# Optimization experiments

Measured on AMD Instinct MI355X. Metric: run time of the kernel, lower is better.

## Reference

```python
import jax, jax.numpy as jnp
import numpy as np

VOCAB, D = 10000, 32
QUEUE_LEN = 100


def setup_inputs() -> dict:
    key = jax.random.key(0)
    ks = jax.random.split(key, 8)
    B, T = 64, 1024
    s = 0.1
    return dict(
        inputs=jax.random.randint(ks[0], (B, T), 0, 10000, dtype=jnp.int32),
        emb=jax.random.normal(ks[1], (VOCAB, D), dtype=jnp.float32) * s,
        k_lstm=jax.random.normal(ks[2], (D, 4 * D), dtype=jnp.float32) * s,
        rk_lstm=jax.random.normal(ks[3], (D, 4 * D), dtype=jnp.float32) * s,
        b_lstm=jnp.zeros((4 * D,), dtype=jnp.float32),
        W1=jax.random.normal(ks[4], (D, D), dtype=jnp.float32) * s,
        b1=jnp.zeros((D,), dtype=jnp.float32),
        W2=jax.random.normal(ks[5], (D, 1), dtype=jnp.float32) * s,
        b2=jnp.zeros((1,), dtype=jnp.float32),
    )


def _lstm(x, k, rk, b):
    # Keras LSTM, gate order [i, f, g(cell), o], sigmoid recurrent act, tanh act.
    B, T, D = x.shape
    xg = jnp.einsum('btd,de->bte', x, k) + b  # precompute input projections

    def step(carry, xg_t):
        h, c = carry
        z = xg_t + h @ rk
        i, f, g, o = jnp.split(z, 4, axis=-1)
        c = jax.nn.sigmoid(f) * c + jax.nn.sigmoid(i) * jnp.tanh(g)
        h = jax.nn.sigmoid(o) * jnp.tanh(c)
        return (h, c), h

    init = (jnp.zeros((B, D), x.dtype), jnp.zeros((B, D), x.dtype))
    _, hs = jax.lax.scan(step, init, jnp.swapaxes(xg, 0, 1))  # [T,B,D]
    return jnp.swapaxes(hs, 0, 1)  # [B,T,D]


def _zero_index_queue(x_ids):
    # Vectorized replacement of the (i,j) Python scan: last QUEUE_LEN positions
    # (row-major order) where token==0, as [QUEUE_LEN,2] int32, padded with -1.
    B, T = x_ids.shape
    flat = (x_ids == 0).reshape(-1)
    N = flat.shape[0]
    ridx = jnp.nonzero(flat[::-1], size=QUEUE_LEN, fill_value=-1)[0]
    pos = jnp.where(ridx >= 0, N - 1 - ridx, -1)[::-1]  # ascending, like deque
    ii = jnp.where(pos >= 0, pos // T, -1)
    jj = jnp.where(pos >= 0, pos % T, -1)
    return jnp.stack([ii, jj], axis=-1).astype(jnp.int32)


def _forward_float(x_ids, emb, k_lstm, rk_lstm, b_lstm, W1, b1, W2, b2):
    x = emb[x_ids]                                  # [B,T,D]
    h = _lstm(x, k_lstm, rk_lstm, b_lstm)           # [B,T,D]
    scores = jnp.einsum('btd,bsd->bts', h, h)       # unscaled dot attention
    attn = jax.nn.softmax(scores, axis=-1)
    ctx = jnp.einsum('bts,bsd->btd', attn, h)       # Keras Attention output
    y = jnp.einsum('btd,bte->bde', ctx, h)          # Dot(axes=(1,1)) -> [B,D,D]
    y = jax.nn.relu(y @ W1 + b1)
    return jax.nn.sigmoid(y @ W2 + b2)              # [B,D,1]


def reference(inputs, emb, k_lstm, rk_lstm, b_lstm, W1, b1, W2, b2):
    x_ids = jnp.where(inputs < VOCAB, inputs, 0)
    out = _forward_float(x_ids, emb, k_lstm, rk_lstm, b_lstm, W1, b1, W2, b2)
    return out, _zero_index_queue(x_ids)
```

## Files before the change

kernel.cpp:

```cpp
#include <hip/hip_runtime.h>
#include <math.h>

#define BB 64
#define TT 1024
#define DD 32
#define GG 128
#define VOCABN 10000
#define QLEN 100

typedef short short8 __attribute__((ext_vector_type(8)));
typedef float floatx4 __attribute__((ext_vector_type(4)));
typedef float floatx2 __attribute__((ext_vector_type(2)));
typedef unsigned short u16;

__device__ __forceinline__ float fsig(float x) {
    return __builtin_amdgcn_rcpf(1.0f + __expf(-x));
}
__device__ __forceinline__ float readlane_f(float v, int l) {
    return __int_as_float(__builtin_amdgcn_readlane(__float_as_int(v), l));
}
__device__ __forceinline__ u16 f2bf_rne(float x) {
    unsigned u = __float_as_uint(x);
    u += 0x7FFF + ((u >> 16) & 1);
    return (u16)(u >> 16);
}
__device__ __forceinline__ float bf2f(u16 s) {
    return __uint_as_float(((unsigned)s) << 16);
}
__device__ __forceinline__ floatx2 fma2(float s, floatx2 w, floatx2 acc) {
    return __builtin_elementwise_fma((floatx2){s, s}, w, acc);
}

#define UU 8
__global__
__attribute__((amdgpu_flat_work_group_size(128, 128)))
__attribute__((amdgpu_waves_per_eu(1, 1)))
void k_lstm_scan(const int* __restrict__ ids,
                 const float* __restrict__ emb,
                 const float* __restrict__ klstm,
                 const float* __restrict__ bias,
                 const float* __restrict__ rk,
                 u16* __restrict__ hh, u16* __restrict__ hl,
                 u16* __restrict__ th, u16* __restrict__ tl,
                 int* __restrict__ list,
                 float* __restrict__ outq) {
    const int b = blockIdx.x;
    const int tid = threadIdx.x;
    const int wv = tid >> 6;
    const int l = tid & 63;
    if (b >= BB) {
        if (wv != 0) return;
        const int4* v4 = (const int4*)ids;
        const int C4 = (BB * TT) / 4 / 64;
        const int b4 = l * C4;
        int cnt = 0;
#pragma unroll 4
        for (int i = 0; i < C4; ++i) {
            int4 v = v4[b4 + i];
            cnt += (v.x == 0 || (unsigned)v.x >= VOCABN);
            cnt += (v.y == 0 || (unsigned)v.y >= VOCABN);
            cnt += (v.z == 0 || (unsigned)v.z >= VOCABN);
            cnt += (v.w == 0 || (unsigned)v.w >= VOCABN);
        }
        int scan = cnt;
#pragma unroll
        for (int o = 1; o < 64; o <<= 1) {
            int nn = __shfl_up(scan, o);
            if (l >= o) scan += nn;
        }
        const int total = __shfl(scan, 63);
        int off = scan - cnt;
        const int base = l * (C4 * 4);
#pragma unroll 4
        for (int i = 0; i < C4; ++i) {
            int4 v = v4[b4 + i];
            if (v.x == 0 || (unsigned)v.x >= VOCABN) list[off++] = base + 4 * i;
            if (v.y == 0 || (unsigned)v.y >= VOCABN) list[off++] = base + 4 * i + 1;
            if (v.z == 0 || (unsigned)v.z >= VOCABN) list[off++] = base + 4 * i + 2;
            if (v.w == 0 || (unsigned)v.w >= VOCABN) list[off++] = base + 4 * i + 3;
        }
        __threadfence();
        const int Kc = total < QLEN ? total : QLEN;
        for (int t = l; t < QLEN; t += 64) {
            float ii = -1.0f, jj = -1.0f;
            if (t >= QLEN - Kc) {
                int pos = list[total - QLEN + t];
                ii = (float)(pos >> 10);
                jj = (float)(pos & (TT - 1));
            }
            outq[2 * t] = ii;
            outq[2 * t + 1] = jj;
        }
        return;
    }

    __shared__ float ring[2][UU][GG];
    __shared__ __align__(16) float hring[2][UU][DD];
    const int* idsb = ids + b * TT;

    if (wv == 1) {
        const int ja = l, jb = l + 64;
        floatx2 kp[DD];
#pragma unroll
        for (int d2 = 0; d2 < DD; ++d2)
            kp[d2] = (floatx2){klstm[d2 * GG + ja], klstm[d2 * GG + jb]};
        const floatx2 bj = (floatx2){bias[ja], bias[jb]};
        const int dd = l & 31;
        const int u_r = l >> 3, dc = (l & 7) * 4;
        const int d_c = l & 31, ug = (l >> 5) * 4;
        u16* hhb = hh + (size_t)b * TT * DD;
        u16* hlb = hl + (size_t)b * TT * DD;
        u16* thb = th + (size_t)b * DD * TT;
        u16* tlb = tl + (size_t)b * DD * TT;

#define PROD_TOKEN(SEL, U, EV)                                               \
        {                                                                    \
            floatx2 z0 = bj;                                                 \
            floatx2 z1 = {0.f, 0.f}, z2 = {0.f, 0.f}, z3 = {0.f, 0.f};       \
            _Pragma("unroll")                                                \
            for (int k = 0; k < DD; k += 4) {                                \
                float e0 = readlane_f(EV, k);                                \
                float e1 = readlane_f(EV, k + 1);                            \
                float e2 = readlane_f(EV, k + 2);                            \
                float e3 = readlane_f(EV, k + 3);                            \
                z0 = fma2(e0, kp[k], z0);                                    \
                z1 = fma2(e1, kp[k + 1], z1);                                \
                z2 = fma2(e2, kp[k + 2], z2);                                \
                z3 = fma2(e3, kp[k + 3], z3);                                \
            }                                                                \
            floatx2 zf = (z0 + z1) + (z2 + z3);                              \
            ring[SEL][U][ja] = zf.x;                                         \
            ring[SEL][U][jb] = zf.y;                                         \
        }

#define CVT_CHUNK(HSEL, TC0)                                                 \
        {                                                                    \
            const float4 hv4 = *(const float4*)&hring[HSEL][u_r][dc];        \
            float xr[4] = {hv4.x, hv4.y, hv4.z, hv4.w};                      \
            u16 rh[4], rl[4];                                                \
            _Pragma("unroll")                                                \
            for (int i = 0; i < 4; ++i) {                                    \
                rh[i] = f2bf_rne(xr[i]);                                     \
                rl[i] = f2bf_rne(xr[i] - bf2f(rh[i]));                       \
            }                                                                \
            ushort4 rhv = {rh[0], rh[1], rh[2], rh[3]};                      \
            ushort4 rlv = {rl[0], rl[1], rl[2], rl[3]};                      \
            *(ushort4*)&hhb[(size_t)((TC0) + u_r) * DD + dc] = rhv;          \
            *(ushort4*)&hlb[(size_t)((TC0) + u_r) * DD + dc] = rlv;          \
            u16 ch[4], cl[4];                                                \
            _Pragma("unroll")                                                \
            for (int j = 0; j < 4; ++j) {                                    \
                float x = hring[HSEL][ug + j][d_c];                          \
                ch[j] = f2bf_rne(x);                                         \
                cl[j] = f2bf_rne(x - bf2f(ch[j]));                           \
            }                                                                \
            ushort4 chv = {ch[0], ch[1], ch[2], ch[3]};                      \
            ushort4 clv = {cl[0], cl[1], cl[2], cl[3]};                      \
            *(ushort4*)&thb[(size_t)d_c * TT + (TC0) + ug] = chv;            \
            *(ushort4*)&tlb[(size_t)d_c * TT + (TC0) + ug] = clv;            \
        }

        {
            int id0 = idsb[0]; if ((unsigned)id0 >= VOCABN) id0 = 0;
            float ec = emb[id0 * DD + dd];
#pragma unroll
            for (int u = 0; u < UU; ++u) {
                float en = 0.f;
                if (u + 1 < UU) {
                    int idn = idsb[u + 1]; if ((unsigned)idn >= VOCABN) idn = 0;
                    en = emb[idn * DD + dd];
                }
                PROD_TOKEN(0, u, ec)
                ec = en;
            }
        }
        __syncthreads();
        int sel = 0;
        for (int t0 = 0; t0 < TT; t0 += UU) {
            if (t0 + UU < TT) {
                const int s = sel ^ 1;
                int id0 = idsb[t0 + UU]; if ((unsigned)id0 >= VOCABN) id0 = 0;
                float ec = emb[id0 * DD + dd];
#pragma unroll
                for (int u = 0; u < UU; ++u) {
                    float en = 0.f;
                    if (u + 1 < UU) {
                        int tn = t0 + UU + u + 1;
                        if (tn > TT - 1) tn = TT - 1;
                        int idn = idsb[tn]; if ((unsigned)idn >= VOCABN) idn = 0;
                        en = emb[idn * DD + dd];
                    }
                    PROD_TOKEN(s, u, ec)
                    ec = en;
                }
            }
            if (t0) CVT_CHUNK((t0 / UU - 1) & 1, t0 - UU)
            __syncthreads();
            sel ^= 1;
        }
        CVT_CHUNK(1, TT - UU)
#undef PROD_TOKEN
#undef CVT_CHUNK
        return;
    }

    const int d = l & 31;
    const bool hi = l >= 32;
    const int ga = (hi ? 32 : 0) + d;
    const int gb = (hi ? 96 : 64) + d;
    floatx2 rkp[DD];
#pragma unroll
    for (int k = 0; k < DD; ++k)
        rkp[k] = (floatx2){rk[k * GG + ga], rk[k * GG + gb]};

    float h = 0.0f, c = 0.0f;
    __syncthreads();
    int sel = 0;
    for (int t0 = 0; t0 < TT; t0 += UU) {
        float pa[UU], pb[UU];
#pragma unroll
        for (int u = 0; u < UU; ++u) {
            pa[u] = ring[sel][u][ga];
            pb[u] = ring[sel][u][gb];
        }
#pragma unroll
        for (int u = 0; u < UU; ++u) {
            floatx2 x0 = {pa[u], pb[u]};
            floatx2 x1 = {0.f, 0.f}, x2 = {0.f, 0.f}, x3 = {0.f, 0.f};
#pragma unroll
            for (int k = 0; k < DD; k += 4) {
                float h0 = readlane_f(h, k);
                float h1 = readlane_f(h, k + 1);
                float h2 = readlane_f(h, k + 2);
                float h3 = readlane_f(h, k + 3);
                x0 = fma2(h0, rkp[k],     x0);
                x1 = fma2(h1, rkp[k + 1], x1);
                x2 = fma2(h2, rkp[k + 2], x2);
                x3 = fma2(h3, rkp[k + 3], x3);
            }
            floatx2 zf = (x0 + x1) + (x2 + x3);
            float za = zf.x, zb = zf.y;
            float a = fsig(za);
            float zbm = hi ? zb : 2.0f * zb;
            float s2 = fsig(zbm);
            float bv = hi ? s2 : 2.0f * s2 - 1.0f;
            auto r1 = __builtin_amdgcn_permlane32_swap(
                __float_as_int(bv), __float_as_int(a), false, false);
            auto r2 = __builtin_amdgcn_permlane32_swap(
                __float_as_int(a), __float_as_int(bv), false, false);
            float fg = __int_as_float(r1[0]);
            float og = __int_as_float(r2[0]);
            c = fmaf(fg, c, a * bv);
            float tc = 2.0f * fsig(2.0f * c) - 1.0f;
            h = og * tc;
            if (!hi) hring[sel][u][d] = h;
        }
        __syncthreads();
        sel ^= 1;
    }
}

__global__ __launch_bounds__(512, 1) void k_attn(const u16* __restrict__ hh,
                                                 const u16* __restrict__ hl,
                                                 const u16* __restrict__ th,
                                                 const u16* __restrict__ tl,
                                                 float* __restrict__ ypart) {
    __shared__ __align__(16) char smem[88064];
    const int tid = threadIdx.x;
    const int w = tid >> 6;
    const int wt = w & 3;
    const int kh = w >> 2;
    const int l = tid & 63;
    const int m = l & 15;
    const int g = l >> 4;
    const int b = blockIdx.x & 63;
    const int qt = (blockIdx.x >> 6) * 4 + wt;
    const int q0 = qt * 64;
    const int e0 = kh * 512;
    const size_t rb = (size_t)b * TT * DD;
    const size_t tb = (size_t)b * DD * TT;
    u16* plw = (u16*)(smem + w * 10240);

    const short8 Qh0 = *(const short8*)&hh[rb + (size_t)(q0 + m) * DD + g * 8];
    const short8 Ql0 = *(const short8*)&hl[rb + (size_t)(q0 + m) * DD + g * 8];
    const short8 Qh1 = *(const short8*)&hh[rb + (size_t)(q0 + 16 + m) * DD + g * 8];
    const short8 Ql1 = *(const short8*)&hl[rb + (size_t)(q0 + 16 + m) * DD + g * 8];
    const short8 Qh2 = *(const short8*)&hh[rb + (size_t)(q0 + 32 + m) * DD + g * 8];
    const short8 Ql2 = *(const short8*)&hl[rb + (size_t)(q0 + 32 + m) * DD + g * 8];
    const short8 Qh3 = *(const short8*)&hh[rb + (size_t)(q0 + 48 + m) * DD + g * 8];
    const short8 Ql3 = *(const short8*)&hl[rb + (size_t)(q0 + 48 + m) * DD + g * 8];
    short8 ONES;
#pragma unroll
    for (int j = 0; j < 8; ++j) ONES[j] = (short)0x3F80;

    floatx4 c0 = {0.f, 0.f, 0.f, 0.f}, c1 = {0.f, 0.f, 0.f, 0.f};
    floatx4 c2 = {0.f, 0.f, 0.f, 0.f}, c3 = {0.f, 0.f, 0.f, 0.f};
    floatx4 c4 = {0.f, 0.f, 0.f, 0.f}, c5 = {0.f, 0.f, 0.f, 0.f};
    floatx4 c6 = {0.f, 0.f, 0.f, 0.f}, c7 = {0.f, 0.f, 0.f, 0.f};
    floatx4 la0 = {0.f, 0.f, 0.f, 0.f}, la1 = {0.f, 0.f, 0.f, 0.f};
    floatx4 la2 = {0.f, 0.f, 0.f, 0.f}, la3 = {0.f, 0.f, 0.f, 0.f};

#define S_BLOCK(QH, QL, KH_A, KL_A, KH_B, KL_B, SA, SB)                       \
    SA = __builtin_amdgcn_mfma_f32_16x16x32_bf16(QH, KH_A, SA, 0, 0, 0);      \
    SA = __builtin_amdgcn_mfma_f32_16x16x32_bf16(QH, KL_A, SA, 0, 0, 0);      \
    SA = __builtin_amdgcn_mfma_f32_16x16x32_bf16(QL, KH_A, SA, 0, 0, 0);      \
    SB = __builtin_amdgcn_mfma_f32_16x16x32_bf16(QH, KH_B, SB, 0, 0, 0);      \
    SB = __builtin_amdgcn_mfma_f32_16x16x32_bf16(QH, KL_B, SB, 0, 0, 0);      \
    SB = __builtin_amdgcn_mfma_f32_16x16x32_bf16(QL, KH_B, SB, 0, 0, 0);

#define EXP_STORE(SA, SB, TILE, SLOT)                                         \
    {                                                                         \
        u16* lp = plw + ((TILE) * 2 + (SLOT)) * 640;                          \
        _Pragma("unroll")                                                     \
        for (int r = 0; r < 4; ++r) {                                         \
            lp[(g * 4 + r) * 40 + m]      = f2bf_rne(__expf(SA[r]));          \
            lp[(g * 4 + r) * 40 + 16 + m] = f2bf_rne(__expf(SB[r]));          \
        }                                                                     \
    }

#define SPANEL(KhA, KlA, KhB, KlB, SLOT)                                      \
    {                                                                         \
        floatx4 sA = {0.f, 0.f, 0.f, 0.f}, sB = {0.f, 0.f, 0.f, 0.f};         \
        floatx4 tA = {0.f, 0.f, 0.f, 0.f}, tB = {0.f, 0.f, 0.f, 0.f};         \
        floatx4 uA = {0.f, 0.f, 0.f, 0.f}, uB = {0.f, 0.f, 0.f, 0.f};         \
        floatx4 vA = {0.f, 0.f, 0.f, 0.f}, vB = {0.f, 0.f, 0.f, 0.f};         \
        S_BLOCK(Qh0, Ql0, KhA, KlA, KhB, KlB, sA, sB)                         \
        S_BLOCK(Qh1, Ql1, KhA, KlA, KhB, KlB, tA, tB)                         \
        S_BLOCK(Qh2, Ql2, KhA, KlA, KhB, KlB, uA, uB)                         \
        S_BLOCK(Qh3, Ql3, KhA, KlA, KhB, KlB, vA, vB)                         \
        EXP_STORE(sA, sB, 0, SLOT)                                            \
        EXP_STORE(tA, tB, 1, SLOT)                                            \
        EXP_STORE(uA, uB, 2, SLOT)                                            \
        EXP_STORE(vA, vB, 3, SLOT)                                            \
    }

#define PV_TILE(T, CA, CB, LAc, SLOTP, VH0, VL0, VH1, VL1)                    \
    {                                                                         \
        const short8 P = *(const short8*)&plw[((T) * 2 + (SLOTP)) * 640 + m * 40 + g * 8]; \
        CA  = __builtin_amdgcn_mfma_f32_16x16x32_bf16(P, VH0, CA, 0, 0, 0);   \
        CA  = __builtin_amdgcn_mfma_f32_16x16x32_bf16(P, VL0, CA, 0, 0, 0);   \
        CB  = __builtin_amdgcn_mfma_f32_16x16x32_bf16(P, VH1, CB, 0, 0, 0);   \
        CB  = __builtin_amdgcn_mfma_f32_16x16x32_bf16(P, VL1, CB, 0, 0, 0);   \
        LAc = __builtin_amdgcn_mfma_f32_16x16x32_bf16(P, ONES, LAc, 0, 0, 0); \
    }

#define PV_PANEL(SLOTP, VH0, VL0, VH1, VL1)                                   \
    PV_TILE(0, c0, c1, la0, SLOTP, VH0, VL0, VH1, VL1)                        \
    PV_TILE(1, c2, c3, la1, SLOTP, VH0, VL0, VH1, VL1)                        \
    PV_TILE(2, c4, c5, la2, SLOTP, VH0, VL0, VH1, VL1)                        \
    PV_TILE(3, c6, c7, la3, SLOTP, VH0, VL0, VH1, VL1)

#define LOAD_K(BASE, RA, RLA, RB, RLB)                                        \
    RA  = *(const short8*)&hh[rb + (size_t)((BASE) + m) * DD + g * 8];        \
    RLA = *(const short8*)&hl[rb + (size_t)((BASE) + m) * DD + g * 8];        \
    RB  = *(const short8*)&hh[rb + (size_t)((BASE) + 16 + m) * DD + g * 8];   \
    RLB = *(const short8*)&hl[rb + (size_t)((BASE) + 16 + m) * DD + g * 8];

#define LOAD_V(BASE, RH0, RL0, RH1, RL1)                                      \
    RH0 = *(const short8*)&th[tb + (size_t)m * TT + (BASE) + g * 8];          \
    RL0 = *(const short8*)&tl[tb + (size_t)m * TT + (BASE) + g * 8];          \
    RH1 = *(const short8*)&th[tb + (size_t)(16 + m) * TT + (BASE) + g * 8];   \
    RL1 = *(const short8*)&tl[tb + (size_t)(16 + m) * TT + (BASE) + g * 8];

    {
        short8 KA, KLA, KB, KLB;
        LOAD_K(e0, KA, KLA, KB, KLB)
        SPANEL(KA, KLA, KB, KLB, 0)
    }
    short8 Vh0, Vl0, Vh1, Vl1, KhA, KlA, KhB, KlB;
    LOAD_V(e0, Vh0, Vl0, Vh1, Vl1)
    LOAD_K(e0 + 32, KhA, KlA, KhB, KlB)

#pragma unroll 1
    for (int j = 1; j < 16; ++j) {
        const int knK = (j < 15) ? e0 + 32 * (j + 1) : 0;
        const int knV = e0 + 32 * j;
        short8 nKhA, nKlA, nKhB, nKlB, nVh0, nVl0, nVh1, nVl1;
        LOAD_K(knK, nKhA, nKlA, nKhB, nKlB)
        LOAD_V(knV, nVh0, nVl0, nVh1, nVl1)

        SPANEL(KhA, KlA, KhB, KlB, j & 1)
        PV_PANEL((j - 1) & 1, Vh0, Vl0, Vh1, Vl1)

        KhA = nKhA; KlA = nKlA; KhB = nKhB; KlB = nKlB;
        Vh0 = nVh0; Vl0 = nVl0; Vh1 = nVh1; Vl1 = nVl1;
    }
    PV_PANEL(1, Vh0, Vl0, Vh1, Vl1)
#undef S_BLOCK
#undef EXP_STORE
#undef SPANEL
#undef PV_TILE
#undef PV_PANEL
#undef LOAD_K

    __syncthreads();
    if (w >= 4) {
        floatx4* dst = (floatx4*)(smem + wt * 13312 + l * 208);
        dst[0] = c0;  dst[1] = c1;  dst[2] = c2;  dst[3] = c3;
        dst[4] = c4;  dst[5] = c5;  dst[6] = c6;  dst[7] = c7;
        dst[8] = la0; dst[9] = la1; dst[10] = la2; dst[11] = la3;
    }
    __syncthreads();
    if (w >= 4) return;
    {
        const floatx4* src = (const floatx4*)(smem + wt * 13312 + l * 208);
        c0 += src[0];  c1 += src[1];  c2 += src[2];  c3 += src[3];
        c4 += src[4];  c5 += src[5];  c6 += src[6];  c7 += src[7];
        la0 += src[8]; la1 += src[9]; la2 += src[10]; la3 += src[11];
    }

    float (*ct)[34] = (float (*)[34])(smem + 53248 + w * 8704);
#pragma unroll
    for (int r = 0; r < 4; ++r) {
        float li0 = __builtin_amdgcn_rcpf(la0[r]);
        float li1 = __builtin_amdgcn_rcpf(la1[r]);
        float li2 = __builtin_amdgcn_rcpf(la2[r]);
        float li3 = __builtin_amdgcn_rcpf(la3[r]);
        ct[g * 4 + r][m]            = c0[r] * li0;
        ct[g * 4 + r][16 + m]       = c1[r] * li0;
        ct[16 + g * 4 + r][m]       = c2[r] * li1;
        ct[16 + g * 4 + r][16 + m]  = c3[r] * li1;
        ct[32 + g * 4 + r][m]       = c4[r] * li2;
        ct[32 + g * 4 + r][16 + m]  = c5[r] * li2;
        ct[48 + g * 4 + r][m]       = c6[r] * li3;
        ct[48 + g * 4 + r][16 + m]  = c7[r] * li3;
    }

    floatx4 y00 = {0.f, 0.f, 0.f, 0.f}, y01 = {0.f, 0.f, 0.f, 0.f};
    floatx4 y10 = {0.f, 0.f, 0.f, 0.f}, y11 = {0.f, 0.f, 0.f, 0.f};
#pragma unroll
    for (int ch = 0; ch < 2; ++ch) {
        const int tloc = ch * 32 + g * 8;
        short8 A0h, A0l, A1h, A1l;
#pragma unroll
        for (int j = 0; j < 8; ++j) {
            float v0 = ct[tloc + j][m];
            u16 h0 = f2bf_rne(v0);
            A0h[j] = (short)h0;
            A0l[j] = (short)f2bf_rne(v0 - bf2f(h0));
            float v1 = ct[tloc + j][16 + m];
            u16 h1 = f2bf_rne(v1);
            A1h[j] = (short)h1;
            A1l[j] = (short)f2bf_rne(v1 - bf2f(h1));
        }
        short8 B0h, B0l, B1h, B1l;
        LOAD_V(q0 + ch * 32, B0h, B0l, B1h, B1l)
        y00 = __builtin_amdgcn_mfma_f32_16x16x32_bf16(A0h, B0h, y00, 0, 0, 0);
        y00 = __builtin_amdgcn_mfma_f32_16x16x32_bf16(A0h, B0l, y00, 0, 0, 0);
        y00 = __builtin_amdgcn_mfma_f32_16x16x32_bf16(A0l, B0h, y00, 0, 0, 0);
        y01 = __builtin_amdgcn_mfma_f32_16x16x32_bf16(A0h, B1h, y01, 0, 0, 0);
        y01 = __builtin_amdgcn_mfma_f32_16x16x32_bf16(A0h, B1l, y01, 0, 0, 0);
        y01 = __builtin_amdgcn_mfma_f32_16x16x32_bf16(A0l, B1h, y01, 0, 0, 0);
        y10 = __builtin_amdgcn_mfma_f32_16x16x32_bf16(A1h, B0h, y10, 0, 0, 0);
        y10 = __builtin_amdgcn_mfma_f32_16x16x32_bf16(A1h, B0l, y10, 0, 0, 0);
        y10 = __builtin_amdgcn_mfma_f32_16x16x32_bf16(A1l, B0h, y10, 0, 0, 0);
        y11 = __builtin_amdgcn_mfma_f32_16x16x32_bf16(A1h, B1h, y11, 0, 0, 0);
        y11 = __builtin_amdgcn_mfma_f32_16x16x32_bf16(A1h, B1l, y11, 0, 0, 0);
        y11 = __builtin_amdgcn_mfma_f32_16x16x32_bf16(A1l, B1h, y11, 0, 0, 0);
    }
#undef LOAD_V
    float* yp = ypart + ((size_t)b * 16 + qt) * (DD * DD);
#pragma unroll
    for (int r = 0; r < 4; ++r) {
        yp[(g * 4 + r) * DD + m]            = y00[r];
        yp[(g * 4 + r) * DD + 16 + m]       = y01[r];
        yp[(16 + g * 4 + r) * DD + m]       = y10[r];
        yp[(16 + g * 4 + r) * DD + 16 + m]  = y11[r];
    }
}

__global__ __launch_bounds__(256) void k_tail(const float* __restrict__ ypart,
                                              const float* __restrict__ W1,
                                              const float* __restrict__ b1,
                                              const float* __restrict__ W2,
                                              const float* __restrict__ b2,
                                              float* __restrict__ out) {
    const int b = blockIdx.x;
    const int tid = threadIdx.x;
    const int e = tid & 31;
    const int d4 = (tid >> 5) * 4;
    const float* yb = ypart + (size_t)b * 16 * (DD * DD);
    __shared__ float ys[DD][DD];
#pragma unroll
    for (int r = 0; r < 4; ++r) {
        float s = 0.f;
#pragma unroll
        for (int p = 0; p < 16; ++p)
            s += yb[p * (DD * DD) + (d4 + r) * DD + e];
        ys[d4 + r][e] = s;
    }
    __syncthreads();
    __shared__ float yr[DD][33];
#pragma unroll
    for (int r = 0; r < 4; ++r) {
        float v = b1[e];
#pragma unroll
        for (int ee = 0; ee < DD; ++ee) v += ys[d4 + r][ee] * W1[ee * DD + e];
        yr[d4 + r][e] = fmaxf(v, 0.0f);
    }
    __syncthreads();
    if (tid < DD) {
        float v = b2[0];
#pragma unroll
        for (int ee = 0; ee < DD; ++ee) v += yr[tid][ee] * W2[ee];
        out[b * DD + tid] = 1.0f / (1.0f + expf(-v));
    }
}

extern "C" void kernel_launch(void* const* d_in, const int* in_sizes, int n_in,
                              void* d_out, int out_size, void* d_ws, size_t ws_size,
                              hipStream_t stream) {
    const int* ids   = (const int*)d_in[0];
    const float* emb = (const float*)d_in[1];
    const float* kl  = (const float*)d_in[2];
    const float* rk  = (const float*)d_in[3];
    const float* bl  = (const float*)d_in[4];
    const float* W1  = (const float*)d_in[5];
    const float* b1  = (const float*)d_in[6];
    const float* W2  = (const float*)d_in[7];
    const float* b2  = (const float*)d_in[8];
    float* out = (float*)d_out;

    char* ws = (char*)d_ws;
    const size_t H_ELEMS = (size_t)BB * TT * DD;
    u16* hh   = (u16*)ws;
    u16* hl   = (u16*)(ws + H_ELEMS * 2);
    u16* th   = (u16*)(ws + H_ELEMS * 4);
    u16* tl   = (u16*)(ws + H_ELEMS * 6);
    float* ypart = (float*)(ws + H_ELEMS * 8);
    int* list = (int*)(ws + H_ELEMS * 8 + H_ELEMS * 8);

    k_lstm_scan<<<BB + 1, 128, 0, stream>>>(ids, emb, kl, bl, rk,
                                            hh, hl, th, tl, list, out + BB * DD);
    k_attn<<<BB * 4, 512, 0, stream>>>(hh, hl, th, tl, ypart);
    k_tail<<<BB, 256, 0, stream>>>(ypart, W1, b1, W2, b2, out);
}
```

Baseline: 342.0 us.

## Fuse tail MLP into attention kernel via last-block-done atomic counter

Removes the separate tail kernel launch. Each attention block now counts its completion per batch with an atomic counter, which the scan kernel resets to zero. The last of the four blocks for a batch reduces the partial y tiles and applies the W1/ReLU/W2/sigmoid head in shared memory. This trades one kernel launch and its gap for threadfences and an atomic, plus a serialized tail on the elected block.

```diff
diff --git a/kernel.cpp b/kernel.cpp
--- a/kernel.cpp
+++ b/kernel.cpp
@@ -43,6 +43,7 @@
                  u16* __restrict__ hh, u16* __restrict__ hl,
                  u16* __restrict__ th, u16* __restrict__ tl,
                  int* __restrict__ list,
+                 int* __restrict__ ycnt,
                  float* __restrict__ outq) {
     const int b = blockIdx.x;
     const int tid = threadIdx.x;
@@ -50,6 +51,7 @@
     const int l = tid & 63;
     if (b >= BB) {
         if (wv != 0) return;
+        if (l < BB) ycnt[l] = 0;
         const int4* v4 = (const int4*)ids;
         const int C4 = (BB * TT) / 4 / 64;
         const int b4 = l * C4;
@@ -264,8 +266,15 @@
                                                  const u16* __restrict__ hl,
                                                  const u16* __restrict__ th,
                                                  const u16* __restrict__ tl,
-                                                 float* __restrict__ ypart) {
+                                                 float* __restrict__ ypart,
+                                                 int* __restrict__ ycnt,
+                                                 const float* __restrict__ W1,
+                                                 const float* __restrict__ b1,
+                                                 const float* __restrict__ W2,
+                                                 const float* __restrict__ b2,
+                                                 float* __restrict__ out) {
     __shared__ __align__(16) char smem[88064];
+    __shared__ int elect;
     const int tid = threadIdx.x;
     const int w = tid >> 6;
     const int wt = w & 3;
@@ -401,86 +410,89 @@
         dst[8] = la0; dst[9] = la1; dst[10] = la2; dst[11] = la3;
     }
     __syncthreads();
-    if (w >= 4) return;
-    {
-        const floatx4* src = (const floatx4*)(smem + wt * 13312 + l * 208);
-        c0 += src[0];  c1 += src[1];  c2 += src[2];  c3 += src[3];
-        c4 += src[4];  c5 += src[5];  c6 += src[6];  c7 += src[7];
-        la0 += src[8]; la1 += src[9]; la2 += src[10]; la3 += src[11];
-    }
-
-    float (*ct)[34] = (float (*)[34])(smem + 53248 + w * 8704);
-#pragma unroll
-    for (int r = 0; r < 4; ++r) {
-        float li0 = __builtin_amdgcn_rcpf(la0[r]);
-        float li1 = __builtin_amdgcn_rcpf(la1[r]);
-        float li2 = __builtin_amdgcn_rcpf(la2[r]);
-        float li3 = __builtin_amdgcn_rcpf(la3[r]);
-        ct[g * 4 + r][m]            = c0[r] * li0;
-        ct[g * 4 + r][16 + m]       = c1[r] * li0;
-        ct[16 + g * 4 + r][m]       = c2[r] * li1;
-        ct[16 + g * 4 + r][16 + m]  = c3[r] * li1;
-        ct[32 + g * 4 + r][m]       = c4[r] * li2;
-        ct[32 + g * 4 + r][16 + m]  = c5[r] * li2;
-        ct[48 + g * 4 + r][m]       = c6[r] * li3;
-        ct[48 + g * 4 + r][16 + m]  = c7[r] * li3;
-    }
-
-    floatx4 y00 = {0.f, 0.f, 0.f, 0.f}, y01 = {0.f, 0.f, 0.f, 0.f};
-    floatx4 y10 = {0.f, 0.f, 0.f, 0.f}, y11 = {0.f, 0.f, 0.f, 0.f};
-#pragma unroll
-    for (int ch = 0; ch < 2; ++ch) {
-        const int tloc = ch * 32 + g * 8;
-        short8 A0h, A0l, A1h, A1l;
-#pragma unroll
-        for (int j = 0; j < 8; ++j) {
-            float v0 = ct[tloc + j][m];
-            u16 h0 = f2bf_rne(v0);
-            A0h[j] = (short)h0;
-            A0l[j] = (short)f2bf_rne(v0 - bf2f(h0));
-            float v1 = ct[tloc + j][16 + m];
-            u16 h1 = f2bf_rne(v1);
-            A1h[j] = (short)h1;
-            A1l[j] = (short)f2bf_rne(v1 - bf2f(h1));
-        }
-        short8 B0h, B0l, B1h, B1l;
-        LOAD_V(q0 + ch * 32, B0h, B0l, B1h, B1l)
-        y00 = __builtin_amdgcn_mfma_f32_16x16x32_bf16(A0h, B0h, y00, 0, 0, 0);
-        y00 = __builtin_amdgcn_mfma_f32_16x16x32_bf16(A0h, B0l, y00, 0, 0, 0);
-        y00 = __builtin_amdgcn_mfma_f32_16x16x32_bf16(A0l, B0h, y00, 0, 0, 0);
-        y01 = __builtin_amdgcn_mfma_f32_16x16x32_bf16(A0h, B1h, y01, 0, 0, 0);
-        y01 = __builtin_amdgcn_mfma_f32_16x16x32_bf16(A0h, B1l, y01, 0, 0, 0);
-        y01 = __builtin_amdgcn_mfma_f32_16x16x32_bf16(A0l, B1h, y01, 0, 0, 0);
-        y10 = __builtin_amdgcn_mfma_f32_16x16x32_bf16(A1h, B0h, y10, 0, 0, 0);
-        y10 = __builtin_amdgcn_mfma_f32_16x16x32_bf16(A1h, B0l, y10, 0, 0, 0);
-        y10 = __builtin_amdgcn_mfma_f32_16x16x32_bf16(A1l, B0h, y10, 0, 0, 0);
-        y11 = __builtin_amdgcn_mfma_f32_16x16x32_bf16(A1h, B1h, y11, 0, 0, 0);
-        y11 = __builtin_amdgcn_mfma_f32_16x16x32_bf16(A1h, B1l, y11, 0, 0, 0);
-        y11 = __builtin_amdgcn_mfma_f32_16x16x32_bf16(A1l, B1h, y11, 0, 0, 0);
+    if (w < 4) {
+        {
+            const floatx4* src = (const floatx4*)(smem + wt * 13312 + l * 208);
+            c0 += src[0];  c1 += src[1];  c2 += src[2];  c3 += src[3];
+            c4 += src[4];  c5 += src[5];  c6 += src[6];  c7 += src[7];
+            la0 += src[8]; la1 += src[9]; la2 += src[10]; la3 += src[11];
+        }
+
+        float (*ct)[34] = (float (*)[34])(smem + 53248 + w * 8704);
+#pragma unroll
+        for (int r = 0; r < 4; ++r) {
+            float li0 = __builtin_amdgcn_rcpf(la0[r]);
+            float li1 = __builtin_amdgcn_rcpf(la1[r]);
+            float li2 = __builtin_amdgcn_rcpf(la2[r]);
+            float li3 = __builtin_amdgcn_rcpf(la3[r]);
+            ct[g * 4 + r][m]            = c0[r] * li0;
+            ct[g * 4 + r][16 + m]       = c1[r] * li0;
+            ct[16 + g * 4 + r][m]       = c2[r] * li1;
+            ct[16 + g * 4 + r][16 + m]  = c3[r] * li1;
+            ct[32 + g * 4 + r][m]       = c4[r] * li2;
+            ct[32 + g * 4 + r][16 + m]  = c5[r] * li2;
+            ct[48 + g * 4 + r][m]       = c6[r] * li3;
+            ct[48 + g * 4 + r][16 + m]  = c7[r] * li3;
+        }
+
+        floatx4 y00 = {0.f, 0.f, 0.f, 0.f}, y01 = {0.f, 0.f, 0.f, 0.f};
+        floatx4 y10 = {0.f, 0.f, 0.f, 0.f}, y11 = {0.f, 0.f, 0.f, 0.f};
+#pragma unroll
+        for (int ch = 0; ch < 2; ++ch) {
+            const int tloc = ch * 32 + g * 8;
+            short8 A0h, A0l, A1h, A1l;
+#pragma unroll
+            for (int j = 0; j < 8; ++j) {
+                float v0 = ct[tloc + j][m];
+                u16 h0 = f2bf_rne(v0);
+                A0h[j] = (short)h0;
+                A0l[j] = (short)f2bf_rne(v0 - bf2f(h0));
+                float v1 = ct[tloc + j][16 + m];
+                u16 h1 = f2bf_rne(v1);
+                A1h[j] = (short)h1;
+                A1l[j] = (short)f2bf_rne(v1 - bf2f(h1));
+            }
+            short8 B0h, B0l, B1h, B1l;
+            LOAD_V(q0 + ch * 32, B0h, B0l, B1h, B1l)
+            y00 = __builtin_amdgcn_mfma_f32_16x16x32_bf16(A0h, B0h, y00, 0, 0, 0);
+            y00 = __builtin_amdgcn_mfma_f32_16x16x32_bf16(A0h, B0l, y00, 0, 0, 0);
+            y00 = __builtin_amdgcn_mfma_f32_16x16x32_bf16(A0l, B0h, y00, 0, 0, 0);
+            y01 = __builtin_amdgcn_mfma_f32_16x16x32_bf16(A0h, B1h, y01, 0, 0, 0);
+            y01 = __builtin_amdgcn_mfma_f32_16x16x32_bf16(A0h, B1l, y01, 0, 0, 0);
+            y01 = __builtin_amdgcn_mfma_f32_16x16x32_bf16(A0l, B1h, y01, 0, 0, 0);
+            y10 = __builtin_amdgcn_mfma_f32_16x16x32_bf16(A1h, B0h, y10, 0, 0, 0);
+            y10 = __builtin_amdgcn_mfma_f32_16x16x32_bf16(A1h, B0l, y10, 0, 0, 0);
+            y10 = __builtin_amdgcn_mfma_f32_16x16x32_bf16(A1l, B0h, y10, 0, 0, 0);
+            y11 = __builtin_amdgcn_mfma_f32_16x16x32_bf16(A1h, B1h, y11, 0, 0, 0);
+            y11 = __builtin_amdgcn_mfma_f32_16x16x32_bf16(A1h, B1l, y11, 0, 0, 0);
+            y11 = __builtin_amdgcn_mfma_f32_16x16x32_bf16(A1l, B1h, y11, 0, 0, 0);
+        }
+        float* yp = ypart + ((size_t)b * 16 + qt) * (DD * DD);
+#pragma unroll
+        for (int r = 0; r < 4; ++r) {
+            yp[(g * 4 + r) * DD + m]            = y00[r];
+            yp[(g * 4 + r) * DD + 16 + m]       = y01[r];
+            yp[(16 + g * 4 + r) * DD + m]       = y10[r];
+            yp[(16 + g * 4 + r) * DD + 16 + m]  = y11[r];
+        }
+        __threadfence();
     }
 #undef LOAD_V
-    float* yp = ypart + ((size_t)b * 16 + qt) * (DD * DD);
-#pragma unroll
-    for (int r = 0; r < 4; ++r) {
-        yp[(g * 4 + r) * DD + m]            = y00[r];
-        yp[(g * 4 + r) * DD + 16 + m]       = y01[r];
-        yp[(16 + g * 4 + r) * DD + m]       = y10[r];
-        yp[(16 + g * 4 + r) * DD + 16 + m]  = y11[r];
-    }
-}
-
-__global__ __launch_bounds__(256) void k_tail(const float* __restrict__ ypart,
-                                              const float* __restrict__ W1,
-                                              const float* __restrict__ b1,
-                                              const float* __restrict__ W2,
-                                              const float* __restrict__ b2,
-                                              float* __restrict__ out) {
-    const int b = blockIdx.x;
-    const int tid = threadIdx.x;
+
+    __syncthreads();
+    if (tid == 0) {
+        int old = atomicAdd(&ycnt[b], 1);
+        elect = (old == 3) ? 1 : 0;
+    }
+    __syncthreads();
+    if (!elect || tid >= 256) return;
+
+    __threadfence();
+    float (*ys)[DD] = (float (*)[DD])smem;
+    float (*yr)[DD + 1] = (float (*)[DD + 1])(smem + 4096);
     const int e = tid & 31;
     const int d4 = (tid >> 5) * 4;
     const float* yb = ypart + (size_t)b * 16 * (DD * DD);
-    __shared__ float ys[DD][DD];
 #pragma unroll
     for (int r = 0; r < 4; ++r) {
         float s = 0.f;
@@ -490,7 +502,6 @@
         ys[d4 + r][e] = s;
     }
     __syncthreads();
-    __shared__ float yr[DD][33];
 #pragma unroll
     for (int r = 0; r < 4; ++r) {
         float v = b1[e];
@@ -528,10 +539,12 @@
     u16* th   = (u16*)(ws + H_ELEMS * 4);
     u16* tl   = (u16*)(ws + H_ELEMS * 6);
     float* ypart = (float*)(ws + H_ELEMS * 8);
+    int* ycnt = (int*)(ws + H_ELEMS * 8 + H_ELEMS * 2);
     int* list = (int*)(ws + H_ELEMS * 8 + H_ELEMS * 8);
 
     k_lstm_scan<<<BB + 1, 128, 0, stream>>>(ids, emb, kl, bl, rk,
-                                            hh, hl, th, tl, list, out + BB * DD);
-    k_attn<<<BB * 4, 512, 0, stream>>>(hh, hl, th, tl, ypart);
-    k_tail<<<BB, 256, 0, stream>>>(ypart, W1, b1, W2, b2, out);
-}
+                                            hh, hl, th, tl, list, ycnt,
+                                            out + BB * DD);
+    k_attn<<<BB * 4, 512, 0, stream>>>(hh, hl, th, tl, ypart, ycnt,
+                                       W1, b1, W2, b2, out);
+}
```

After: 373.2 us. 1.09x slower.
